# Kernel optimization log

Hardware: AMD Instinct MI355X
Metric: run time of the kernel (lower is better)

The kernel has to match this reference:

```python
import math
import jax, jax.numpy as jnp
import numpy as np

D, NH, NL, NP = 256, 8, 4, 4
C = D // NH
VALUE_SHAPES = np.array([[128, 128], [64, 64], [32, 32], [16, 16]], dtype=np.int32)


def _offset_bias():
    # Faithful to MSDeformAttn._reset_parameters grid init for sampling_offsets.bias
    th = np.arange(NH, dtype=np.float32) * (2.0 * np.pi / NH)
    g = np.stack([np.cos(th), np.sin(th)], -1)                      # [NH,2]
    g = g / np.abs(g).max(-1, keepdims=True)
    g = np.tile(g[:, None, None, :], (1, NL, NP, 1))                # [NH,NL,NP,2]
    g = g * np.arange(1, NP + 1, dtype=np.float32)[None, None, :, None]
    return jnp.asarray(g.reshape(-1), jnp.float32)


def setup_inputs() -> dict:
    key = jax.random.key(0)
    ks = jax.random.split(key, 10)
    bs, Q = 8, 2048
    LV = int((VALUE_SHAPES[:, 0] * VALUE_SHAPES[:, 1]).sum())
    s = 0.02
    return {
        "query": jax.random.normal(ks[0], (bs, Q, D), jnp.float32),
        "refer_bbox": jax.random.uniform(ks[1], (bs, Q, NL, 2), jnp.float32),
        "value": jax.random.normal(ks[2], (bs, LV, D), jnp.float32),
        "value_shapes": VALUE_SHAPES,  # static numpy (shapes must be compile-time constants)
        "W_value": jax.random.normal(ks[3], (D, D), jnp.float32) * s,
        "b_value": jnp.zeros((D,), jnp.float32),
        "W_off": jax.random.normal(ks[4], (D, NH * NL * NP * 2), jnp.float32) * 0.01,
        "b_off": _offset_bias(),
        "W_attn": jax.random.normal(ks[5], (D, NH * NL * NP), jnp.float32) * s,
        "b_attn": jnp.zeros((NH * NL * NP,), jnp.float32),
        "W_out": jax.random.normal(ks[6], (D, D), jnp.float32) * s,
        "b_out": jnp.zeros((D,), jnp.float32),
    }


def _ms_deform_attn(value, shapes, loc, attn):
    # value: [bs,LV,NH,C], loc: [bs,Q,NH,NL,NP,2] in [0,1], attn: [bs,Q,NH,NL,NP]
    bs, LV = value.shape[:2]
    Q = loc.shape[1]
    BH = bs * NH
    v = value.transpose(0, 2, 1, 3).reshape(BH, LV, C)              # [BH,LV,C]
    loc = loc.transpose(0, 2, 1, 3, 4, 5).reshape(BH, Q, NL, NP, 2)
    attn = attn.transpose(0, 2, 1, 3, 4).reshape(BH, Q, NL, NP)
    acc = jnp.zeros((BH, Q, C), value.dtype)
    start = 0
    for lvl in range(NL):
        H, W = int(shapes[lvl, 0]), int(shapes[lvl, 1])
        img = v[:, start:start + H * W]                             # [BH,HW,C]
        start += H * W
        # grid_sample(align_corners=False): pixel coord = loc * size - 0.5
        x = loc[:, :, lvl, :, 0] * W - 0.5                          # [BH,Q,NP]
        y = loc[:, :, lvl, :, 1] * H - 0.5
        x0 = jnp.floor(x); y0 = jnp.floor(y)
        fx = x - x0; fy = y - y0
        x0i = x0.astype(jnp.int32); y0i = y0.astype(jnp.int32)
        samp = jnp.zeros((BH, Q, NP, C), value.dtype)
        for dx, dy in ((0, 0), (1, 0), (0, 1), (1, 1)):
            xi = x0i + dx; yi = y0i + dy
            valid = (xi >= 0) & (xi < W) & (yi >= 0) & (yi < H)     # zero padding
            w = (fx if dx else 1.0 - fx) * (fy if dy else 1.0 - fy)
            w = jnp.where(valid, w, 0.0)
            idx = jnp.clip(yi, 0, H - 1) * W + jnp.clip(xi, 0, W - 1)
            g = jnp.take_along_axis(img, idx.reshape(BH, Q * NP)[..., None], axis=1)
            samp = samp + w[..., None] * g.reshape(BH, Q, NP, C)
        acc = acc + (samp * attn[:, :, lvl, :, None]).sum(2)
    return acc.reshape(bs, NH, Q, C).transpose(0, 2, 1, 3).reshape(bs, Q, D)


def reference(query, refer_bbox, value, value_shapes, W_value, b_value,
              W_off, b_off, W_attn, b_attn, W_out, b_out):
    shapes = np.asarray(value_shapes)  # static
    bs, Q = query.shape[:2]
    LV = value.shape[1]
    v = (value @ W_value + b_value).reshape(bs, LV, NH, C)
    off = (query @ W_off + b_off).reshape(bs, Q, NH, NL, NP, 2)
    attn = jax.nn.softmax((query @ W_attn + b_attn).reshape(bs, Q, NH, NL * NP), -1)
    attn = attn.reshape(bs, Q, NH, NL, NP)
    norm = jnp.asarray(shapes[:, ::-1], query.dtype)                # (W,H) per level
    loc = refer_bbox[:, :, None, :, None, :] + off / norm[None, None, None, :, None, :]
    out = _ms_deform_attn(v, shapes, loc, attn)
    return out @ W_out + b_out
```

## Files before the change

kernel.cpp:

```cpp
#include <hip/hip_runtime.h>
#include <hip/hip_bf16.h>

#define D_MODEL 256
#define NHEAD   8
#define NLVL    4
#define NPTS    4
#define CH      32
#define QTOT    2048
#define BS      8
#define LVTOT   21760
#define KDIM    256

typedef __attribute__((ext_vector_type(8))) short bf16x8;
typedef __attribute__((ext_vector_type(4))) float f32x4;

__device__ inline float bf_lo(unsigned u) { unsigned t = u << 16; float f; __builtin_memcpy(&f, &t, 4); return f; }
__device__ inline float bf_hi(unsigned u) { unsigned t = u & 0xffff0000u; float f; __builtin_memcpy(&f, &t, 4); return f; }
__device__ inline float bfu2f(unsigned short s) { unsigned t = (unsigned)s << 16; float f; __builtin_memcpy(&f, &t, 4); return f; }
__device__ inline unsigned short f2bfu(float f) { __hip_bfloat16 h = __float2bfloat16(f); unsigned short u; __builtin_memcpy(&u, &h, 2); return u; }

__global__ __launch_bounds__(256)
void convert_W(const float* __restrict__ W, __hip_bfloat16* __restrict__ Wt, int sh) {
    int t = blockIdx.x * 256 + threadIdx.x;
    int k = t >> sh, n = t & ((1 << sh) - 1);
    Wt[n * 256 + k] = __float2bfloat16(W[(k << sh) + n]);
}

__global__ __launch_bounds__(256)
void convert_q(const float* __restrict__ q, __hip_bfloat16* __restrict__ qb) {
    int t = blockIdx.x * 256 + threadIdx.x;
    float4 f = ((const float4*)q)[t];
    __hip_bfloat16 h4[4] = {__float2bfloat16(f.x), __float2bfloat16(f.y),
                            __float2bfloat16(f.z), __float2bfloat16(f.w)};
    ((uint2*)qb)[t] = *(const uint2*)h4;
}

#define BK  64
#define LDP 72
#define LDC 264

__global__ __launch_bounds__(256, 2)
void gemm_value_mfma(const float* __restrict__ A,
                     const __hip_bfloat16* __restrict__ Wt,
                     const float* __restrict__ bias,
                     __hip_bfloat16* __restrict__ v) {
    __shared__ __align__(16) char smem[128 * LDC * 2];
    __hip_bfloat16* As = (__hip_bfloat16*)smem;
    __hip_bfloat16* Bs = (__hip_bfloat16*)(smem + 128 * LDP * 2);
    __hip_bfloat16* Cs = (__hip_bfloat16*)smem;

    const int tid  = threadIdx.x;
    const int lane = tid & 63;
    const int wave = tid >> 6;
    const int wr   = wave >> 1;
    const int wc   = wave & 1;
    const int rowBase = blockIdx.x * 128;

    const int m0   = lane & 15;
    const int quad = lane >> 4;

    const int sr = tid >> 1;
    const int sk = (tid & 1) * 32;

    f32x4 acc[4][8] = {};

    for (int kc = 0; kc < KDIM; kc += BK) {
        const float* ap = A + (size_t)(rowBase + sr) * KDIM + kc + sk;
#pragma unroll
        for (int j = 0; j < 4; ++j) {
            float4 f0 = *(const float4*)(ap + j * 8);
            float4 f1 = *(const float4*)(ap + j * 8 + 4);
            __align__(16) __hip_bfloat16 t8[8];
            t8[0] = __float2bfloat16(f0.x); t8[1] = __float2bfloat16(f0.y);
            t8[2] = __float2bfloat16(f0.z); t8[3] = __float2bfloat16(f0.w);
            t8[4] = __float2bfloat16(f1.x); t8[5] = __float2bfloat16(f1.y);
            t8[6] = __float2bfloat16(f1.z); t8[7] = __float2bfloat16(f1.w);
            *(uint4*)&As[sr * LDP + sk + j * 8] = *(const uint4*)t8;
        }
        const uint4* bp = (const uint4*)(Wt + (size_t)tid * KDIM + kc);
#pragma unroll
        for (int j = 0; j < 8; ++j)
            *(uint4*)&Bs[tid * LDP + j * 8] = bp[j];
        __syncthreads();

#pragma unroll
        for (int ks = 0; ks < 2; ++ks) {
            bf16x8 af[4], bfv[8];
#pragma unroll
            for (int i = 0; i < 4; ++i)
                af[i] = *(const bf16x8*)&As[(wr * 64 + i * 16 + m0) * LDP + ks * 32 + quad * 8];
#pragma unroll
            for (int j = 0; j < 8; ++j)
                bfv[j] = *(const bf16x8*)&Bs[(wc * 128 + j * 16 + m0) * LDP + ks * 32 + quad * 8];
#pragma unroll
            for (int i = 0; i < 4; ++i)
#pragma unroll
                for (int j = 0; j < 8; ++j)
                    acc[i][j] = __builtin_amdgcn_mfma_f32_16x16x32_bf16(af[i], bfv[j], acc[i][j], 0, 0, 0);
        }
        __syncthreads();
    }

    const int b = rowBase / LVTOT;
    const int pixBase = rowBase - b * LVTOT;
#pragma unroll
    for (int j = 0; j < 8; ++j) {
        const int gcol = wc * 128 + j * 16 + m0;
        const float bv = bias[gcol];
#pragma unroll
        for (int i = 0; i < 4; ++i) {
            const int lrow = wr * 64 + i * 16 + quad * 4;
#pragma unroll
            for (int r = 0; r < 4; ++r)
                Cs[(lrow + r) * LDC + gcol] = __float2bfloat16(acc[i][j][r] + bv);
        }
    }
    __syncthreads();

    {
        char* dst = (char*)v + (size_t)(b * LVTOT + pixBase) * 512;
        const char* src = (const char*)Cs;
#pragma unroll
        for (int it = 0; it < 16; ++it) {
            const int o = it * 4096 + tid * 16;
            const int row = o >> 9;
            const int cb  = o & 511;
            uint4 val = *(const uint4*)(src + row * (LDC * 2) + cb);
            *(uint4*)(dst + o) = val;
        }
    }
}

struct StorePlain {
    float* o;
    int ncol;
    __device__ void operator()(int row, int col, float val) const {
        o[(size_t)row * ncol + col] = val;
    }
};

template <typename Store>
__global__ __launch_bounds__(256, 2)
void gemm_bf16_mfma(const __hip_bfloat16* __restrict__ A,
                    const __hip_bfloat16* __restrict__ Wt,
                    const float* __restrict__ bias, Store store) {
    __shared__ __align__(16) __hip_bfloat16 As[128 * LDP];
    __shared__ __align__(16) __hip_bfloat16 Bs[128 * LDP];

    const int tid  = threadIdx.x;
    const int lane = tid & 63;
    const int wave = tid >> 6;
    const int rowBase = blockIdx.x * 128;
    const int cb = blockIdx.y * 128;

    const int m0   = lane & 15;
    const int quad = lane >> 4;

    const int sr = tid >> 1;
    const int sk = (tid & 1) * 32;

    f32x4 acc[2][8] = {};

    for (int kc = 0; kc < KDIM; kc += BK) {
        const uint4* ap = (const uint4*)(A + (size_t)(rowBase + sr) * KDIM + kc + sk);
#pragma unroll
        for (int j = 0; j < 4; ++j)
            *(uint4*)&As[sr * LDP + sk + j * 8] = ap[j];
        const uint4* bp = (const uint4*)(Wt + (size_t)(cb + sr) * KDIM + kc + sk);
#pragma unroll
        for (int j = 0; j < 4; ++j)
            *(uint4*)&Bs[sr * LDP + sk + j * 8] = bp[j];
        __syncthreads();

#pragma unroll
        for (int ks = 0; ks < 2; ++ks) {
            bf16x8 af[2], bfv[8];
#pragma unroll
            for (int i = 0; i < 2; ++i)
                af[i] = *(const bf16x8*)&As[(wave * 32 + i * 16 + m0) * LDP + ks * 32 + quad * 8];
#pragma unroll
            for (int j = 0; j < 8; ++j)
                bfv[j] = *(const bf16x8*)&Bs[(j * 16 + m0) * LDP + ks * 32 + quad * 8];
#pragma unroll
            for (int i = 0; i < 2; ++i)
#pragma unroll
                for (int j = 0; j < 8; ++j)
                    acc[i][j] = __builtin_amdgcn_mfma_f32_16x16x32_bf16(af[i], bfv[j], acc[i][j], 0, 0, 0);
        }
        __syncthreads();
    }

#pragma unroll
    for (int j = 0; j < 8; ++j) {
        const int col = cb + j * 16 + m0;
        const float bv = bias[col];
#pragma unroll
        for (int i = 0; i < 2; ++i) {
            const int row0 = rowBase + wave * 32 + i * 16 + quad * 4;
#pragma unroll
            for (int r = 0; r < 4; ++r)
                store(row0 + r, col, acc[i][j][r] + bv);
        }
    }
}

__global__ __launch_bounds__(256)
void sample_kernel(const float* __restrict__ off_ws,
                   const float* __restrict__ logits_ws,
                   const float* __restrict__ bbox,
                   const __hip_bfloat16* __restrict__ v,
                   __hip_bfloat16* __restrict__ acc_bf) {
    __shared__ __align__(16) float off_s[8 * 256];
    __shared__ __align__(16) float attn_s[8 * 128];
    __shared__ float bbox_s[64];
    __shared__ __align__(16) int idx_s[1024 * 4];
    __shared__ __align__(8) unsigned short w_s[1024 * 4];

    const int tid = threadIdx.x;
    const int b = blockIdx.x & 7;
    const int gq0 = b * QTOT + (blockIdx.x >> 3) * 8;

    const float4* osrc = (const float4*)(off_ws + (size_t)gq0 * 256);
    ((float4*)off_s)[tid] = osrc[tid];
    ((float4*)off_s)[tid + 256] = osrc[tid + 256];
    const float4* lsrc = (const float4*)(logits_ws + (size_t)gq0 * 128);
    ((float4*)attn_s)[tid] = lsrc[tid];
    if (tid < 64) bbox_s[tid] = bbox[(size_t)gq0 * 8 + tid];
    __syncthreads();

    if (tid < 64) {
        int qq = tid >> 3, h = tid & 7;
        float* p = attn_s + qq * 128 + h * 16;
        float m = p[0];
#pragma unroll
        for (int i = 1; i < 16; ++i) m = fmaxf(m, p[i]);
        float e[16], s = 0.f;
#pragma unroll
        for (int i = 0; i < 16; ++i) { e[i] = __expf(p[i] - m); s += e[i]; }
        float inv = 1.f / s;
#pragma unroll
        for (int i = 0; i < 16; ++i) p[i] = e[i] * inv;
    }
    __syncthreads();

#pragma unroll
    for (int r = 0; r < 4; ++r) {
        const int tap = tid + r * 256;
        const int qq = tap >> 7, h = (tap >> 4) & 7, l = (tap >> 2) & 3, p = tap & 3;
        const int Wd = 128 >> l;
        const int st = (l == 0) ? 0 : (l == 1) ? 16384 : (l == 2) ? 20480 : 21504;

        const float bx = bbox_s[qq * 8 + l * 2 + 0];
        const float by = bbox_s[qq * 8 + l * 2 + 1];
        const float ox = off_s[qq * 256 + h * 32 + l * 8 + p * 2 + 0];
        const float oy = off_s[qq * 256 + h * 32 + l * 8 + p * 2 + 1];
        const float att = attn_s[qq * 128 + h * 16 + l * 4 + p];

        const float x = bx * (float)Wd + ox - 0.5f;
        const float y = by * (float)Wd + oy - 0.5f;
        const float x0f = floorf(x), y0f = floorf(y);
        const float fx = x - x0f, fy = y - y0f;
        const int x0 = (int)x0f, y0 = (int)y0f;
        const int x1 = x0 + 1, y1 = y0 + 1;
        const bool vx0 = (unsigned)x0 < (unsigned)Wd;
        const bool vx1 = (unsigned)x1 < (unsigned)Wd;
        const bool vy0 = (unsigned)y0 < (unsigned)Wd;
        const bool vy1 = (unsigned)y1 < (unsigned)Wd;
        const int cx0 = min(max(x0, 0), Wd - 1), cx1 = min(max(x1, 0), Wd - 1);
        const int cy0 = min(max(y0, 0), Wd - 1), cy1 = min(max(y1, 0), Wd - 1);

        int4 idx;
        idx.x = (st + cy0 * Wd + cx0) << 9;
        idx.y = (st + cy0 * Wd + cx1) << 9;
        idx.z = (st + cy1 * Wd + cx0) << 9;
        idx.w = (st + cy1 * Wd + cx1) << 9;
        float w0 = (vx0 && vy0) ? (1.f - fx) * (1.f - fy) * att : 0.f;
        float w1 = (vx1 && vy0) ? fx * (1.f - fy) * att : 0.f;
        float w2 = (vx0 && vy1) ? (1.f - fx) * fy * att : 0.f;
        float w3 = (vx1 && vy1) ? fx * fy * att : 0.f;

        *(int4*)&idx_s[tap * 4] = idx;
        unsigned short w4[4] = {f2bfu(w0), f2bfu(w1), f2bfu(w2), f2bfu(w3)};
        *(uint2*)&w_s[tap * 4] = *(const uint2*)w4;
    }
    __syncthreads();

    const int lane = tid & 63;
    const int wave = tid >> 6;
    const int g = lane >> 4;
    const int c2 = lane & 15;

    const char* vbase = (const char*)v + (size_t)b * LVTOT * 512 + c2 * 4;

    for (int i = 0; i < 16; ++i) {
        const int pair = wave * 16 + i;
        const int qq = pair >> 3, hh = pair & 7;
        const char* slab = vbase + hh * 64;
        const int tbase = qq * 128 + hh * 16;

        float ax0 = 0.f, ay0 = 0.f, ax1 = 0.f, ay1 = 0.f, ax2 = 0.f, ay2 = 0.f, ax3 = 0.f, ay3 = 0.f;
#pragma unroll
        for (int ts = 0; ts < 4; ++ts) {
            const int tap = tbase + ts * 4 + g;
            const int4 idx = *(const int4*)&idx_s[tap * 4];
            const ushort4 ww = *(const ushort4*)&w_s[tap * 4];
            unsigned u0 = *(const unsigned*)(slab + idx.x);
            unsigned u1 = *(const unsigned*)(slab + idx.y);
            unsigned u2 = *(const unsigned*)(slab + idx.z);
            unsigned u3 = *(const unsigned*)(slab + idx.w);
            float w0 = bfu2f(ww.x), w1 = bfu2f(ww.y), w2 = bfu2f(ww.z), w3 = bfu2f(ww.w);
            ax0 += w0 * bf_lo(u0); ay0 += w0 * bf_hi(u0);
            ax1 += w1 * bf_lo(u1); ay1 += w1 * bf_hi(u1);
            ax2 += w2 * bf_lo(u2); ay2 += w2 * bf_hi(u2);
            ax3 += w3 * bf_lo(u3); ay3 += w3 * bf_hi(u3);
        }
        float sx = (ax0 + ax1) + (ax2 + ax3);
        float sy = (ay0 + ay1) + (ay2 + ay3);
        sx += __shfl_xor(sx, 16); sy += __shfl_xor(sy, 16);
        sx += __shfl_xor(sx, 32); sy += __shfl_xor(sy, 32);
        if (g == 0) {
            __hip_bfloat16 h2[2] = {__float2bfloat16(sx), __float2bfloat16(sy)};
            unsigned packed; __builtin_memcpy(&packed, h2, 4);
            *(unsigned*)((char*)acc_bf + ((size_t)(gq0 + qq) * 256 + hh * 32 + c2 * 2) * 2) = packed;
        }
    }
}

extern "C" void kernel_launch(void* const* d_in, const int* in_sizes, int n_in,
                              void* d_out, int out_size, void* d_ws, size_t ws_size,
                              hipStream_t stream) {
    const float* query   = (const float*)d_in[0];
    const float* bbox    = (const float*)d_in[1];
    const float* value   = (const float*)d_in[2];
    const float* W_value = (const float*)d_in[4];
    const float* b_value = (const float*)d_in[5];
    const float* W_off   = (const float*)d_in[6];
    const float* b_off   = (const float*)d_in[7];
    const float* W_attn  = (const float*)d_in[8];
    const float* b_attn  = (const float*)d_in[9];
    const float* W_out   = (const float*)d_in[10];
    const float* b_out   = (const float*)d_in[11];
    float* out = (float*)d_out;

    char* ws = (char*)d_ws;
    __hip_bfloat16* v_ws  = (__hip_bfloat16*)ws;
    float* off_ws         = (float*)(ws + 89128960);
    float* logits_ws      = (float*)(ws + 89128960 + 16777216);
    __hip_bfloat16* acc_bf = (__hip_bfloat16*)(ws + 89128960 + 16777216 + 8388608);
    __hip_bfloat16* q_bf   = (__hip_bfloat16*)(ws + 89128960 + 16777216 + 8388608 + 8388608);

    __hip_bfloat16* Wt_v    = acc_bf;
    __hip_bfloat16* Wt_off  = acc_bf + 65536;
    __hip_bfloat16* Wt_attn = acc_bf + 131072;
    __hip_bfloat16* Wt_out  = q_bf;

    const int NQ = BS * QTOT;
    const int NVROWS = BS * LVTOT;

    convert_q<<<NQ * KDIM / 1024, 256, 0, stream>>>(query, q_bf);
    convert_W<<<256, 256, 0, stream>>>(W_value, Wt_v, 8);
    convert_W<<<256, 256, 0, stream>>>(W_off, Wt_off, 8);
    convert_W<<<128, 256, 0, stream>>>(W_attn, Wt_attn, 7);

    gemm_value_mfma<<<NVROWS / 128, 256, 0, stream>>>(value, Wt_v, b_value, v_ws);

    gemm_bf16_mfma<<<dim3(NQ / 128, 2), 256, 0, stream>>>(
        q_bf, Wt_off, b_off, StorePlain{off_ws, 256});

    gemm_bf16_mfma<<<dim3(NQ / 128, 1), 256, 0, stream>>>(
        q_bf, Wt_attn, b_attn, StorePlain{logits_ws, 128});

    convert_W<<<256, 256, 0, stream>>>(W_out, Wt_out, 8);

    sample_kernel<<<NQ / 8, 256, 0, stream>>>(off_ws, logits_ws, bbox, v_ws, acc_bf);

    gemm_bf16_mfma<<<dim3(NQ / 128, 2), 256, 0, stream>>>(
        acc_bf, Wt_out, b_out, StorePlain{out, 256});
}
```

Before: 408.5 us.

## Prefetch next K-tile into registers in GEMMs and halve value-GEMM LDS footprint

Both MFMA GEMM kernels now issue global loads for the next K chunk into registers before running the MFMAs on the current chunk, then write them to LDS after a barrier. This overlaps global memory latency with compute. The value GEMM epilogue now stages its output tile in two 64-row halves, so shared memory shrinks to the A+B tile size. That may allow more blocks per CU, at the cost of higher register pressure from the prefetch buffers and extra barriers.

```diff
diff --git a/kernel.cpp b/kernel.cpp
--- a/kernel.cpp
+++ b/kernel.cpp
@@ -44,7 +44,7 @@
                      const __hip_bfloat16* __restrict__ Wt,
                      const float* __restrict__ bias,
                      __hip_bfloat16* __restrict__ v) {
-    __shared__ __align__(16) char smem[128 * LDC * 2];
+    __shared__ __align__(16) char smem[128 * LDP * 2 + 256 * LDP * 2];
     __hip_bfloat16* As = (__hip_bfloat16*)smem;
     __hip_bfloat16* Bs = (__hip_bfloat16*)(smem + 128 * LDP * 2);
     __hip_bfloat16* Cs = (__hip_bfloat16*)smem;
@@ -62,26 +62,51 @@
     const int sr = tid >> 1;
     const int sk = (tid & 1) * 32;
 
+    const float* aRow = A + (size_t)(rowBase + sr) * KDIM + sk;
+    const __hip_bfloat16* bRow = Wt + (size_t)tid * KDIM;
+
     f32x4 acc[4][8] = {};
-
-    for (int kc = 0; kc < KDIM; kc += BK) {
-        const float* ap = A + (size_t)(rowBase + sr) * KDIM + kc + sk;
-#pragma unroll
-        for (int j = 0; j < 4; ++j) {
-            float4 f0 = *(const float4*)(ap + j * 8);
-            float4 f1 = *(const float4*)(ap + j * 8 + 4);
-            __align__(16) __hip_bfloat16 t8[8];
-            t8[0] = __float2bfloat16(f0.x); t8[1] = __float2bfloat16(f0.y);
-            t8[2] = __float2bfloat16(f0.z); t8[3] = __float2bfloat16(f0.w);
-            t8[4] = __float2bfloat16(f1.x); t8[5] = __float2bfloat16(f1.y);
-            t8[6] = __float2bfloat16(f1.z); t8[7] = __float2bfloat16(f1.w);
-            *(uint4*)&As[sr * LDP + sk + j * 8] = *(const uint4*)t8;
-        }
-        const uint4* bp = (const uint4*)(Wt + (size_t)tid * KDIM + kc);
-#pragma unroll
-        for (int j = 0; j < 8; ++j)
-            *(uint4*)&Bs[tid * LDP + j * 8] = bp[j];
-        __syncthreads();
+    float4 aPf[8];
+    uint4  bPf[8];
+
+#pragma unroll
+    for (int j = 0; j < 4; ++j) {
+        aPf[2 * j]     = *(const float4*)(aRow + j * 8);
+        aPf[2 * j + 1] = *(const float4*)(aRow + j * 8 + 4);
+    }
+    {
+        const uint4* bp = (const uint4*)bRow;
+#pragma unroll
+        for (int j = 0; j < 8; ++j) bPf[j] = bp[j];
+    }
+#pragma unroll
+    for (int j = 0; j < 4; ++j) {
+        __align__(16) __hip_bfloat16 t8[8];
+        float4 f0 = aPf[2 * j], f1 = aPf[2 * j + 1];
+        t8[0] = __float2bfloat16(f0.x); t8[1] = __float2bfloat16(f0.y);
+        t8[2] = __float2bfloat16(f0.z); t8[3] = __float2bfloat16(f0.w);
+        t8[4] = __float2bfloat16(f1.x); t8[5] = __float2bfloat16(f1.y);
+        t8[6] = __float2bfloat16(f1.z); t8[7] = __float2bfloat16(f1.w);
+        *(uint4*)&As[sr * LDP + sk + j * 8] = *(const uint4*)t8;
+    }
+#pragma unroll
+    for (int j = 0; j < 8; ++j)
+        *(uint4*)&Bs[tid * LDP + j * 8] = bPf[j];
+    __syncthreads();
+
+#pragma unroll
+    for (int it = 0; it < 4; ++it) {
+        if (it < 3) {
+            const float* ap = aRow + (it + 1) * BK;
+#pragma unroll
+            for (int j = 0; j < 4; ++j) {
+                aPf[2 * j]     = *(const float4*)(ap + j * 8);
+                aPf[2 * j + 1] = *(const float4*)(ap + j * 8 + 4);
+            }
+            const uint4* bp = (const uint4*)(bRow + (it + 1) * BK);
+#pragma unroll
+            for (int j = 0; j < 8; ++j) bPf[j] = bp[j];
+        }
 
 #pragma unroll
         for (int ks = 0; ks < 2; ++ks) {
@@ -99,35 +124,55 @@
                     acc[i][j] = __builtin_amdgcn_mfma_f32_16x16x32_bf16(af[i], bfv[j], acc[i][j], 0, 0, 0);
         }
         __syncthreads();
+
+        if (it < 3) {
+#pragma unroll
+            for (int j = 0; j < 4; ++j) {
+                __align__(16) __hip_bfloat16 t8[8];
+                float4 f0 = aPf[2 * j], f1 = aPf[2 * j + 1];
+                t8[0] = __float2bfloat16(f0.x); t8[1] = __float2bfloat16(f0.y);
+                t8[2] = __float2bfloat16(f0.z); t8[3] = __float2bfloat16(f0.w);
+                t8[4] = __float2bfloat16(f1.x); t8[5] = __float2bfloat16(f1.y);
+                t8[6] = __float2bfloat16(f1.z); t8[7] = __float2bfloat16(f1.w);
+                *(uint4*)&As[sr * LDP + sk + j * 8] = *(const uint4*)t8;
+            }
+#pragma unroll
+            for (int j = 0; j < 8; ++j)
+                *(uint4*)&Bs[tid * LDP + j * 8] = bPf[j];
+            __syncthreads();
+        }
     }
 
     const int b = rowBase / LVTOT;
     const int pixBase = rowBase - b * LVTOT;
 #pragma unroll
-    for (int j = 0; j < 8; ++j) {
-        const int gcol = wc * 128 + j * 16 + m0;
-        const float bv = bias[gcol];
-#pragma unroll
-        for (int i = 0; i < 4; ++i) {
-            const int lrow = wr * 64 + i * 16 + quad * 4;
-#pragma unroll
-            for (int r = 0; r < 4; ++r)
-                Cs[(lrow + r) * LDC + gcol] = __float2bfloat16(acc[i][j][r] + bv);
-        }
-    }
-    __syncthreads();
-
-    {
-        char* dst = (char*)v + (size_t)(b * LVTOT + pixBase) * 512;
+    for (int half = 0; half < 2; ++half) {
+        if (wr == half) {
+#pragma unroll
+            for (int j = 0; j < 8; ++j) {
+                const int gcol = wc * 128 + j * 16 + m0;
+                const float bv = bias[gcol];
+#pragma unroll
+                for (int i = 0; i < 4; ++i) {
+                    const int lrow = i * 16 + quad * 4;
+#pragma unroll
+                    for (int r = 0; r < 4; ++r)
+                        Cs[(lrow + r) * LDC + gcol] = __float2bfloat16(acc[i][j][r] + bv);
+                }
+            }
+        }
+        __syncthreads();
+        char* dst = (char*)v + (size_t)(b * LVTOT + pixBase + half * 64) * 512;
         const char* src = (const char*)Cs;
 #pragma unroll
-        for (int it = 0; it < 16; ++it) {
-            const int o = it * 4096 + tid * 16;
+        for (int itr = 0; itr < 8; ++itr) {
+            const int o = itr * 4096 + tid * 16;
             const int row = o >> 9;
             const int cb  = o & 511;
             uint4 val = *(const uint4*)(src + row * (LDC * 2) + cb);
             *(uint4*)(dst + o) = val;
         }
+        if (half == 0) __syncthreads();
     }
 }
 
@@ -159,18 +204,33 @@
     const int sr = tid >> 1;
     const int sk = (tid & 1) * 32;
 
+    const __hip_bfloat16* aRow = A + (size_t)(rowBase + sr) * KDIM + sk;
+    const __hip_bfloat16* bRow = Wt + (size_t)(cb + sr) * KDIM + sk;
+
     f32x4 acc[2][8] = {};
-
-    for (int kc = 0; kc < KDIM; kc += BK) {
-        const uint4* ap = (const uint4*)(A + (size_t)(rowBase + sr) * KDIM + kc + sk);
-#pragma unroll
-        for (int j = 0; j < 4; ++j)
-            *(uint4*)&As[sr * LDP + sk + j * 8] = ap[j];
-        const uint4* bp = (const uint4*)(Wt + (size_t)(cb + sr) * KDIM + kc + sk);
-#pragma unroll
-        for (int j = 0; j < 4; ++j)
-            *(uint4*)&Bs[sr * LDP + sk + j * 8] = bp[j];
-        __syncthreads();
+    uint4 aPf[4], bPf[4];
+
+    {
+        const uint4* ap = (const uint4*)aRow;
+        const uint4* bp = (const uint4*)bRow;
+#pragma unroll
+        for (int j = 0; j < 4; ++j) { aPf[j] = ap[j]; bPf[j] = bp[j]; }
+    }
+#pragma unroll
+    for (int j = 0; j < 4; ++j) {
+        *(uint4*)&As[sr * LDP + sk + j * 8] = aPf[j];
+        *(uint4*)&Bs[sr * LDP + sk + j * 8] = bPf[j];
+    }
+    __syncthreads();
+
+#pragma unroll
+    for (int it = 0; it < 4; ++it) {
+        if (it < 3) {
+            const uint4* ap = (const uint4*)(aRow + (it + 1) * BK);
+            const uint4* bp = (const uint4*)(bRow + (it + 1) * BK);
+#pragma unroll
+            for (int j = 0; j < 4; ++j) { aPf[j] = ap[j]; bPf[j] = bp[j]; }
+        }
 
 #pragma unroll
         for (int ks = 0; ks < 2; ++ks) {
@@ -188,6 +248,15 @@
                     acc[i][j] = __builtin_amdgcn_mfma_f32_16x16x32_bf16(af[i], bfv[j], acc[i][j], 0, 0, 0);
         }
         __syncthreads();
+
+        if (it < 3) {
+#pragma unroll
+            for (int j = 0; j < 4; ++j) {
+                *(uint4*)&As[sr * LDP + sk + j * 8] = aPf[j];
+                *(uint4*)&Bs[sr * LDP + sk + j * 8] = bPf[j];
+            }
+            __syncthreads();
+        }
     }
 
 #pragma unroll
```

Result: slower. 481.8 us (+17.9%).
